# Kernel optimization log

Measured on AMD Instinct MI355X. Metric: run time of the kernel, lower is better.

The kernel has to match this reference:

```python
import jax, jax.numpy as jnp
import numpy as np

BN_EPS = 1e-5


def setup_inputs() -> dict:
    key = jax.random.key(0)
    ks = jax.random.split(key, 4)
    B, N, D = 8, 8192, 256
    outD = 256
    s = 1.0 / np.sqrt(D)
    return {
        "feature": jax.random.normal(ks[0], (B, N, D), dtype=jnp.float32),
        "W_qk": jax.random.normal(ks[1], (2, D, D), dtype=jnp.float32) * s,
        "b_qk": jnp.zeros((2, D), dtype=jnp.float32),
        "W_v": jax.random.normal(ks[2], (D, outD), dtype=jnp.float32) * s,
        "b_v": jnp.zeros((outD,), dtype=jnp.float32),
        "gamma": jnp.ones((D,), dtype=jnp.float32),
        "beta": jnp.zeros((D,), dtype=jnp.float32),
    }


def reference(feature, W_qk, b_qk, W_v, b_v, gamma, beta):
    # QK: [B, 2, N, D]
    QK = jnp.einsum("bnd,kde->bkne", feature, W_qk) + b_qk[None, :, None, :]
    # value: [B, N, outD]
    value = jnp.einsum("bnd,de->bne", feature, W_v) + b_v
    query = QK[:, 0]  # [B, N, D]
    key = QK[:, 1]    # [B, N, D]
    # softmax over the sequence axis (dim=1), per (batch, channel)
    sm = jax.nn.softmax(key, axis=1)
    # lambda context: softmax^T @ value -> [B, D, outD]
    lam = jnp.einsum("bnd,bne->bde", sm, value)
    # BatchNorm1d(featureDim) in training mode: channel axis = D (axis 1),
    # stats over (batch, spatial) = axes (0, 2); biased variance as torch uses.
    mean = jnp.mean(lam, axis=(0, 2), keepdims=True)
    var = jnp.var(lam, axis=(0, 2), keepdims=True)
    bn = (lam - mean) * jax.lax.rsqrt(var + BN_EPS)
    bn = bn * gamma[None, :, None] + beta[None, :, None]
    # result: query @ BN -> [B, N, outD]
    return jnp.einsum("bnd,bde->bne", query, bn)
```

## Files before the change

### kernel.cpp

```cpp
#include <hip/hip_runtime.h>

typedef unsigned short u16;
typedef __bf16 bf16x8 __attribute__((ext_vector_type(8)));
typedef float f32x4 __attribute__((ext_vector_type(4)));

#define LOG2E 1.44269504088896f

__device__ inline u16 f2b(float f) {
    unsigned u = __float_as_uint(f);
    u += 0x7fff + ((u >> 16) & 1);
    return (u16)(u >> 16);
}
__device__ inline float b2f(u16 u) { return __uint_as_float(((unsigned)u) << 16); }
__device__ inline unsigned pk2(float a, float b) {
    return (unsigned)f2b(a) | ((unsigned)f2b(b) << 16);
}
__device__ inline uint4 pack8(float4 a, float4 b) {
    return uint4{pk2(a.x, a.y), pk2(a.z, a.w), pk2(b.x, b.y), pk2(b.z, b.w)};
}

__device__ inline f32x4 mfma_bf16(uint4 a, uint4 b, f32x4 c) {
    return __builtin_amdgcn_mfma_f32_16x16x32_bf16(
        __builtin_bit_cast(bf16x8, a), __builtin_bit_cast(bf16x8, b), c, 0, 0, 0);
}

__global__ __launch_bounds__(256) void prep_w(const float* __restrict__ Wqk,
                                              const float* __restrict__ Wv,
                                              u16* __restrict__ WkT,
                                              u16* __restrict__ WvT,
                                              u16* __restrict__ Wqb) {
    int idx = blockIdx.x * 256 + threadIdx.x;
    int which = idx >> 16;
    int i = (idx >> 8) & 255;
    int j = idx & 255;
    if (which == 0)
        WkT[i * 256 + j] = f2b(Wqk[65536 + j * 256 + i]);
    else if (which == 1)
        WvT[i * 256 + j] = f2b(Wv[j * 256 + i]);
    else
        Wqb[i * 256 + j] = f2b(Wqk[i * 256 + j]);
}

__global__ __launch_bounds__(256) void gemm_kv(const float* __restrict__ A,
                                               const u16* __restrict__ BtK,
                                               const u16* __restrict__ BtV,
                                               const float* __restrict__ biasK,
                                               const float* __restrict__ biasV,
                                               u16* __restrict__ KT,
                                               u16* __restrict__ VT,
                                               u16* __restrict__ Xb) {
    __shared__ __align__(16) u16 lds[9216];
    u16* As = lds;
    u16* BsK = lds + 3072;
    u16* BsV = lds + 6144;

    const int t = threadIdx.x;
    const int c0 = blockIdx.x * 64;
    const int r0 = blockIdx.y * 64;

    const int tr = t >> 2;
    const int tk = (t & 3) * 8;
    const int w = t >> 6;
    const int lane = t & 63;
    const int l15 = lane & 15;
    const int q = lane >> 4;

    f32x4 accK[4], accV[4];
#pragma unroll
    for (int c = 0; c < 4; ++c) {
        accK[c] = f32x4{0.f, 0.f, 0.f, 0.f};
        accV[c] = f32x4{0.f, 0.f, 0.f, 0.f};
    }

    const float* Arow = A + (long)(r0 + tr) * 256 + tk;
    const u16* BrowK = BtK + (long)(c0 + tr) * 256 + tk;
    const u16* BrowV = BtV + (long)(c0 + tr) * 256 + tk;
    u16* AsW = &As[tr * 48 + tk];
    u16* BsWK = &BsK[tr * 48 + tk];
    u16* BsWV = &BsV[tr * 48 + tk];
    const u16* AsR = &As[(w * 16 + l15) * 48 + q * 8];
    const u16* BsRK = &BsK[l15 * 48 + q * 8];
    const u16* BsRV = &BsV[l15 * 48 + q * 8];
    const bool writeX = (Xb != nullptr) && (blockIdx.x == 0);
    u16* XbW = Xb + (long)(r0 + tr) * 256 + tk;

    float4 a0 = ((const float4*)Arow)[0];
    float4 a1 = ((const float4*)Arow)[1];
    uint4 bk = *(const uint4*)BrowK;
    uint4 bvv = *(const uint4*)BrowV;

    for (int k0 = 0; k0 < 256; k0 += 32) {
        uint4 ap = pack8(a0, a1);
        *(uint4*)AsW = ap;
        *(uint4*)BsWK = bk;
        *(uint4*)BsWV = bvv;
        if (writeX) *(uint4*)(XbW + k0) = ap;
        __syncthreads();
        if (k0 + 32 < 256) {
            a0 = ((const float4*)(Arow + k0 + 32))[0];
            a1 = ((const float4*)(Arow + k0 + 32))[1];
            bk = *(const uint4*)(BrowK + k0 + 32);
            bvv = *(const uint4*)(BrowV + k0 + 32);
        }
        uint4 af = *(const uint4*)AsR;
#pragma unroll
        for (int c = 0; c < 4; ++c) {
            uint4 bfK = *(const uint4*)(BsRK + c * 16 * 48);
            uint4 bfV = *(const uint4*)(BsRV + c * 16 * 48);
            accK[c] = mfma_bf16(af, bfK, accK[c]);
            accV[c] = mfma_bf16(af, bfV, accV[c]);
        }
        __syncthreads();
    }

    u16* Ct = lds;
    const int bb = r0 >> 13;
    const int n0 = r0 & 8191;
    const int cc = t >> 2;
    const int ng = (t & 3) * 16;
#pragma unroll
    for (int pass = 0; pass < 2; ++pass) {
        const f32x4* acc = pass ? accV : accK;
        const float* bias = pass ? biasV : biasK;
        u16* CT = pass ? VT : KT;
#pragma unroll
        for (int c = 0; c < 4; ++c) {
            float bv = bias[c0 + c * 16 + l15];
#pragma unroll
            for (int r = 0; r < 4; ++r) {
                Ct[(c * 16 + l15) * 72 + (w * 16 + q * 4 + r)] = f2b(acc[c][r] + bv);
            }
        }
        __syncthreads();
        long off = ((long)bb * 256 + (c0 + cc)) * 8192 + n0 + ng;
        uint4 v0 = *(uint4*)&Ct[cc * 72 + ng];
        uint4 v1 = *(uint4*)&Ct[cc * 72 + ng + 8];
        *(uint4*)(CT + off) = v0;
        *(uint4*)(CT + off + 8) = v1;
        __syncthreads();
    }
}

template <bool A_F32, bool OUT_F32, bool BIAS>
__global__ __launch_bounds__(256) void gemm_rowC(const void* __restrict__ Ain,
                                                 const u16* __restrict__ Bt,
                                                 const float* __restrict__ bias,
                                                 void* __restrict__ Cout,
                                                 int K, int rowsPerBatch, long btStride) {
    __shared__ __align__(16) u16 As[64 * 48];
    __shared__ __align__(16) u16 Bs[64 * 48];

    const int t = threadIdx.x;
    const int c0 = blockIdx.x * 64;
    const int r0 = blockIdx.y * 64;
    const int bb = r0 / rowsPerBatch;
    const u16* BtB = Bt + (long)bb * btStride;

    const int tr = t >> 2;
    const int tk = (t & 3) * 8;
    const int w = t >> 6;
    const int lane = t & 63;
    const int l15 = lane & 15;
    const int q = lane >> 4;

    f32x4 acc[4];
#pragma unroll
    for (int c = 0; c < 4; ++c) acc[c] = f32x4{0.f, 0.f, 0.f, 0.f};

    const float* ArowF = (const float*)Ain + (long)(r0 + tr) * K + tk;
    const u16* ArowB = (const u16*)Ain + (long)(r0 + tr) * K + tk;
    const u16* Brow = BtB + (long)(c0 + tr) * K + tk;
    u16* AsW = &As[tr * 48 + tk];
    u16* BsW = &Bs[tr * 48 + tk];
    const u16* AsR = &As[(w * 16 + l15) * 48 + q * 8];
    const u16* BsR = &Bs[l15 * 48 + q * 8];

    uint4 av;
    float4 a0, a1;
    if (A_F32) {
        a0 = ((const float4*)ArowF)[0];
        a1 = ((const float4*)ArowF)[1];
    } else {
        av = *(const uint4*)ArowB;
    }
    uint4 bv = *(const uint4*)Brow;

    for (int k0 = 0; k0 < K; k0 += 32) {
        *(uint4*)AsW = A_F32 ? pack8(a0, a1) : av;
        *(uint4*)BsW = bv;
        __syncthreads();
        if (k0 + 32 < K) {
            if (A_F32) {
                a0 = ((const float4*)(ArowF + k0 + 32))[0];
                a1 = ((const float4*)(ArowF + k0 + 32))[1];
            } else {
                av = *(const uint4*)(ArowB + k0 + 32);
            }
            bv = *(const uint4*)(Brow + k0 + 32);
        }
        uint4 af = *(const uint4*)AsR;
#pragma unroll
        for (int c = 0; c < 4; ++c) {
            uint4 bf = *(const uint4*)(BsR + c * 16 * 48);
            acc[c] = mfma_bf16(af, bf, acc[c]);
        }
        __syncthreads();
    }

#pragma unroll
    for (int c = 0; c < 4; ++c) {
        int col = c0 + c * 16 + l15;
        float bv2 = 0.f;
        if (BIAS) bv2 = bias[(long)bb * 256 + col];
#pragma unroll
        for (int r = 0; r < 4; ++r) {
            int row = r0 + w * 16 + q * 4 + r;
            float v = acc[c][r] + bv2;
            if (OUT_F32)
                ((float*)Cout)[(long)row * 256 + col] = v;
            else
                ((u16*)Cout)[(long)row * 256 + col] = f2b(v);
        }
    }
}

__global__ __launch_bounds__(256) void gemm_splitk(const u16* __restrict__ VT,
                                                   const u16* __restrict__ PT,
                                                   float* __restrict__ lamP,
                                                   int chunk) {
    __shared__ __align__(16) u16 As[64 * 48];
    __shared__ __align__(16) u16 Bs[64 * 48];

    const int t = threadIdx.x;
    const int c0 = blockIdx.x * 64;
    const int r0 = blockIdx.y * 64;
    const int s = blockIdx.z;
    const int bb = r0 >> 8;
    const long n0 = (long)s * chunk;

    const int tr = t >> 2;
    const int tk = (t & 3) * 8;
    const int w = t >> 6;
    const int lane = t & 63;
    const int l15 = lane & 15;
    const int q = lane >> 4;

    f32x4 acc[4];
#pragma unroll
    for (int c = 0; c < 4; ++c) acc[c] = f32x4{0.f, 0.f, 0.f, 0.f};

    const u16* Arow = VT + (long)(r0 + tr) * 8192 + n0 + tk;
    const u16* Brow = PT + ((long)bb * 256 + c0 + tr) * 8192 + n0 + tk;
    u16* AsW = &As[tr * 48 + tk];
    u16* BsW = &Bs[tr * 48 + tk];
    const u16* AsR = &As[(w * 16 + l15) * 48 + q * 8];
    const u16* BsR = &Bs[l15 * 48 + q * 8];

    uint4 av = *(const uint4*)Arow;
    uint4 bv = *(const uint4*)Brow;

    for (int k0 = 0; k0 < chunk; k0 += 32) {
        *(uint4*)AsW = av;
        *(uint4*)BsW = bv;
        __syncthreads();
        if (k0 + 32 < chunk) {
            av = *(const uint4*)(Arow + k0 + 32);
            bv = *(const uint4*)(Brow + k0 + 32);
        }
        uint4 af = *(const uint4*)AsR;
#pragma unroll
        for (int c = 0; c < 4; ++c) {
            uint4 bf = *(const uint4*)(BsR + c * 16 * 48);
            acc[c] = mfma_bf16(af, bf, acc[c]);
        }
        __syncthreads();
    }

    float* outp = lamP + (long)s * 524288;
#pragma unroll
    for (int c = 0; c < 4; ++c) {
        int col = c0 + c * 16 + l15;
#pragma unroll
        for (int r = 0; r < 4; ++r) {
            int row = r0 + w * 16 + q * 4 + r;
            outp[(long)row * 256 + col] = acc[c][r];
        }
    }
}

__global__ __launch_bounds__(256) void reduce_lam(const float* __restrict__ lamP,
                                                  float* __restrict__ lamT, int S) {
    int i = blockIdx.x * 256 + threadIdx.x;
    float4 v = ((const float4*)lamP)[i];
    for (int s = 1; s < S; ++s) {
        float4 p = ((const float4*)(lamP + (long)s * 524288))[i];
        v.x += p.x; v.y += p.y; v.z += p.z; v.w += p.w;
    }
    ((float4*)lamT)[i] = v;
}

__global__ __launch_bounds__(64) void softmax_rows(u16* __restrict__ KT) {
    const int row = blockIdx.x;
    const int lane = threadIdx.x;
    u16* p = KT + (long)row * 8192;

    uint4 buf[16];
#pragma unroll
    for (int i = 0; i < 16; ++i) buf[i] = *(const uint4*)(p + (i * 64 + lane) * 8);

    float m = -1e30f;
#pragma unroll
    for (int i = 0; i < 16; ++i) {
        const unsigned* u = (const unsigned*)&buf[i];
#pragma unroll
        for (int j = 0; j < 4; ++j) {
            m = fmaxf(m, fmaxf(b2f((u16)(u[j] & 0xffff)), b2f((u16)(u[j] >> 16))));
        }
    }
#pragma unroll
    for (int s = 32; s > 0; s >>= 1) m = fmaxf(m, __shfl_xor(m, s, 64));

    float sum = 0.f;
#pragma unroll
    for (int i = 0; i < 16; ++i) {
        const unsigned* u = (const unsigned*)&buf[i];
#pragma unroll
        for (int j = 0; j < 4; ++j) {
            sum += exp2f((b2f((u16)(u[j] & 0xffff)) - m) * LOG2E);
            sum += exp2f((b2f((u16)(u[j] >> 16)) - m) * LOG2E);
        }
    }
#pragma unroll
    for (int s = 32; s > 0; s >>= 1) sum += __shfl_xor(sum, s, 64);
    float rl = 1.0f / sum;

#pragma unroll
    for (int i = 0; i < 16; ++i) {
        unsigned* u = (unsigned*)&buf[i];
#pragma unroll
        for (int j = 0; j < 4; ++j) {
            float a = exp2f((b2f((u16)(u[j] & 0xffff)) - m) * LOG2E) * rl;
            float b = exp2f((b2f((u16)(u[j] >> 16)) - m) * LOG2E) * rl;
            u[j] = (unsigned)f2b(a) | ((unsigned)f2b(b) << 16);
        }
        *(uint4*)(p + (i * 64 + lane) * 8) = buf[i];
    }
}

__global__ __launch_bounds__(256) void bn_kernel(const float* __restrict__ lamT,
                                                 const float* __restrict__ gamma,
                                                 const float* __restrict__ beta,
                                                 u16* __restrict__ bnT) {
    const int d = blockIdx.x;
    const int t = threadIdx.x;
    float vals[8];
    float s = 0.f, ss = 0.f;
#pragma unroll
    for (int i = 0; i < 8; ++i) {
        float v = lamT[(long)(i * 256 + t) * 256 + d];
        vals[i] = v;
        s += v;
        ss += v * v;
    }
#pragma unroll
    for (int sh = 32; sh > 0; sh >>= 1) {
        s += __shfl_xor(s, sh, 64);
        ss += __shfl_xor(ss, sh, 64);
    }
    __shared__ float red[8];
    int w = t >> 6;
    if ((t & 63) == 0) {
        red[w] = s;
        red[w + 4] = ss;
    }
    __syncthreads();
    s = red[0] + red[1] + red[2] + red[3];
    ss = red[4] + red[5] + red[6] + red[7];
    float mean = s * (1.f / 2048.f);
    float var = ss * (1.f / 2048.f) - mean * mean;
    float scale = gamma[d] * rsqrtf(var + 1e-5f);
    float shift = beta[d] - mean * scale;
#pragma unroll
    for (int i = 0; i < 8; ++i)
        bnT[(long)(i * 256 + t) * 256 + d] = f2b(vals[i] * scale + shift);
}

__global__ __launch_bounds__(256) void outb_kernel(const float* __restrict__ bq,
                                                   const u16* __restrict__ bnT,
                                                   float* __restrict__ outb) {
    int b = blockIdx.x, e = threadIdx.x;
    const u16* rowp = bnT + ((long)b * 256 + e) * 256;
    float s = 0.f;
    for (int dd = 0; dd < 256; ++dd) s += bq[dd] * b2f(rowp[dd]);
    outb[b * 256 + e] = s;
}

extern "C" void kernel_launch(void* const* d_in, const int* in_sizes, int n_in,
                              void* d_out, int out_size, void* d_ws, size_t ws_size,
                              hipStream_t stream) {
    const float* feat = (const float*)d_in[0];
    const float* W_qk = (const float*)d_in[1];
    const float* b_qk = (const float*)d_in[2];
    const float* W_v = (const float*)d_in[3];
    const float* b_v = (const float*)d_in[4];
    const float* gamma = (const float*)d_in[5];
    const float* beta = (const float*)d_in[6];
    float* out = (float*)d_out;

    char* ws = (char*)d_ws;
    u16* KT = (u16*)(ws);
    u16* VT = (u16*)(ws + 33554432);
    u16* WkT = (u16*)(ws + 67108864);
    u16* WvT = (u16*)(ws + 67239936);
    u16* Wqb = (u16*)(ws + 67371008);
    const size_t base = 67502080;
    float* lamP = (float*)(ws + base);
    size_t avail = (ws_size > base) ? ws_size - base : 0;
    int S = (avail >= 8u * 2097152u) ? 8 : ((avail >= 4u * 2097152u) ? 4 : 2);
    u16* Xb = nullptr;
    if (avail >= (size_t)S * 2097152u + 33554432u) Xb = (u16*)(ws + base + (size_t)S * 2097152u);
    float* lamT = (float*)ws;
    u16* bnT = (u16*)(ws + 2097152);
    u16* WfoldT = (u16*)(ws + 3145728);
    float* outb = (float*)(ws + 4194304);

    prep_w<<<768, 256, 0, stream>>>(W_qk, W_v, WkT, WvT, Wqb);
    gemm_kv<<<dim3(4, 1024), 256, 0, stream>>>(feat, WkT, WvT, b_qk + 256, b_v, KT, VT, Xb);
    softmax_rows<<<2048, 64, 0, stream>>>(KT);
    gemm_splitk<<<dim3(4, 32, S), 256, 0, stream>>>(VT, KT, lamP, 8192 / S);
    reduce_lam<<<512, 256, 0, stream>>>(lamP, lamT, S);
    bn_kernel<<<256, 256, 0, stream>>>(lamT, gamma, beta, bnT);
    outb_kernel<<<8, 256, 0, stream>>>(b_qk, bnT, outb);
    gemm_rowC<false, false, false><<<dim3(4, 32), 256, 0, stream>>>(bnT, Wqb, nullptr,
                                                                    WfoldT, 256, 2048, 0L);
    if (Xb)
        gemm_rowC<false, true, true><<<dim3(4, 1024), 256, 0, stream>>>(Xb, WfoldT, outb, out,
                                                                        256, 8192, 65536L);
    else
        gemm_rowC<true, true, true><<<dim3(4, 1024), 256, 0, stream>>>(feat, WfoldT, outb, out,
                                                                       256, 8192, 65536L);
}
```

Baseline: 289.3 us.

## Widen GEMM tiles to full 256 columns and load B tiles via global_load_lds

Several GEMM kernels are restructured at once. gemm_kv and gemm_out now give each block all 256 output columns, so the fp32 feature rows are read and packed once instead of four times, and the bf16 Xb copy is dropped. gemm_splitk moves to 128x128 tiles with more split-K slices, and B tiles (and A tiles where already bf16) are loaded straight into LDS with global_load_lds. The trade is much higher register pressure (32 accumulator vectors in gemm_kv), unpadded LDS rows that may cause bank conflicts, and a larger partial-sum buffer to reduce.

```diff
diff --git a/kernel.cpp b/kernel.cpp
--- a/kernel.cpp
+++ b/kernel.cpp
@@ -18,10 +18,14 @@
 __device__ inline uint4 pack8(float4 a, float4 b) {
     return uint4{pk2(a.x, a.y), pk2(a.z, a.w), pk2(b.x, b.y), pk2(b.z, b.w)};
 }
-
 __device__ inline f32x4 mfma_bf16(uint4 a, uint4 b, f32x4 c) {
     return __builtin_amdgcn_mfma_f32_16x16x32_bf16(
         __builtin_bit_cast(bf16x8, a), __builtin_bit_cast(bf16x8, b), c, 0, 0, 0);
+}
+__device__ inline void ld16(const u16* g, u16* l) {
+    __builtin_amdgcn_global_load_lds(
+        (const __attribute__((address_space(1))) unsigned int*)g,
+        (__attribute__((address_space(3))) unsigned int*)l, 16, 0, 0);
 }
 
 __global__ __launch_bounds__(256) void prep_w(const float* __restrict__ Wqk,
@@ -41,251 +45,202 @@
         Wqb[i * 256 + j] = f2b(Wqk[i * 256 + j]);
 }
 
-__global__ __launch_bounds__(256) void gemm_kv(const float* __restrict__ A,
-                                               const u16* __restrict__ BtK,
-                                               const u16* __restrict__ BtV,
-                                               const float* __restrict__ biasK,
-                                               const float* __restrict__ biasV,
-                                               u16* __restrict__ KT,
-                                               u16* __restrict__ VT,
-                                               u16* __restrict__ Xb) {
-    __shared__ __align__(16) u16 lds[9216];
+__global__ __launch_bounds__(256, 2) void gemm_kv(const float* __restrict__ A,
+                                                  const u16* __restrict__ BtK,
+                                                  const u16* __restrict__ BtV,
+                                                  const float* __restrict__ biasK,
+                                                  const float* __restrict__ biasV,
+                                                  u16* __restrict__ KT,
+                                                  u16* __restrict__ VT) {
+    __shared__ __align__(16) u16 lds[18432];
     u16* As = lds;
-    u16* BsK = lds + 3072;
-    u16* BsV = lds + 6144;
+    u16* BsK = lds + 2048;
+    u16* BsV = lds + 10240;
 
     const int t = threadIdx.x;
-    const int c0 = blockIdx.x * 64;
-    const int r0 = blockIdx.y * 64;
-
-    const int tr = t >> 2;
-    const int tk = (t & 3) * 8;
-    const int w = t >> 6;
-    const int lane = t & 63;
-    const int l15 = lane & 15;
-    const int q = lane >> 4;
-
-    f32x4 accK[4], accV[4];
-#pragma unroll
-    for (int c = 0; c < 4; ++c) {
+    const int r0 = blockIdx.x * 64;
+    const int w = t >> 6, lane = t & 63, l15 = lane & 15, q = lane >> 4;
+
+    f32x4 accK[16], accV[16];
+#pragma unroll
+    for (int c = 0; c < 16; ++c) {
         accK[c] = f32x4{0.f, 0.f, 0.f, 0.f};
         accV[c] = f32x4{0.f, 0.f, 0.f, 0.f};
     }
 
-    const float* Arow = A + (long)(r0 + tr) * 256 + tk;
-    const u16* BrowK = BtK + (long)(c0 + tr) * 256 + tk;
-    const u16* BrowV = BtV + (long)(c0 + tr) * 256 + tk;
-    u16* AsW = &As[tr * 48 + tk];
-    u16* BsWK = &BsK[tr * 48 + tk];
-    u16* BsWV = &BsV[tr * 48 + tk];
-    const u16* AsR = &As[(w * 16 + l15) * 48 + q * 8];
-    const u16* BsRK = &BsK[l15 * 48 + q * 8];
-    const u16* BsRV = &BsV[l15 * 48 + q * 8];
-    const bool writeX = (Xb != nullptr) && (blockIdx.x == 0);
-    u16* XbW = Xb + (long)(r0 + tr) * 256 + tk;
+    const int ar = t >> 2;
+    const int ak = (t & 3) * 8;
+    const float* Arow = A + (long)(r0 + ar) * 256 + ak;
+    u16* AsW = As + t * 8;
 
     float4 a0 = ((const float4*)Arow)[0];
     float4 a1 = ((const float4*)Arow)[1];
-    uint4 bk = *(const uint4*)BrowK;
-    uint4 bvv = *(const uint4*)BrowV;
 
     for (int k0 = 0; k0 < 256; k0 += 32) {
-        uint4 ap = pack8(a0, a1);
-        *(uint4*)AsW = ap;
-        *(uint4*)BsWK = bk;
-        *(uint4*)BsWV = bvv;
-        if (writeX) *(uint4*)(XbW + k0) = ap;
+#pragma unroll
+        for (int j = 0; j < 4; ++j) {
+            int ch = j * 256 + t;
+            int br = ch >> 2;
+            int bk = (ch & 3) * 8;
+            ld16(BtK + br * 256 + k0 + bk, BsK + j * 2048 + w * 512);
+            ld16(BtV + br * 256 + k0 + bk, BsV + j * 2048 + w * 512);
+        }
+        *(uint4*)AsW = pack8(a0, a1);
         __syncthreads();
         if (k0 + 32 < 256) {
             a0 = ((const float4*)(Arow + k0 + 32))[0];
             a1 = ((const float4*)(Arow + k0 + 32))[1];
-            bk = *(const uint4*)(BrowK + k0 + 32);
-            bvv = *(const uint4*)(BrowV + k0 + 32);
-        }
-        uint4 af = *(const uint4*)AsR;
-#pragma unroll
-        for (int c = 0; c < 4; ++c) {
-            uint4 bfK = *(const uint4*)(BsRK + c * 16 * 48);
-            uint4 bfV = *(const uint4*)(BsRV + c * 16 * 48);
-            accK[c] = mfma_bf16(af, bfK, accK[c]);
-            accV[c] = mfma_bf16(af, bfV, accV[c]);
-        }
-        __syncthreads();
-    }
-
+        }
+        uint4 af = *(const uint4*)(As + (w * 16 + l15) * 32 + q * 8);
+#pragma unroll
+        for (int c = 0; c < 16; ++c) {
+            uint4 bK = *(const uint4*)(BsK + (c * 16 + l15) * 32 + q * 8);
+            uint4 bV = *(const uint4*)(BsV + (c * 16 + l15) * 32 + q * 8);
+            accK[c] = mfma_bf16(af, bK, accK[c]);
+            accV[c] = mfma_bf16(af, bV, accV[c]);
+        }
+        __syncthreads();
+    }
+
+    const int bb = r0 >> 13, n0 = r0 & 8191;
     u16* Ct = lds;
-    const int bb = r0 >> 13;
-    const int n0 = r0 & 8191;
-    const int cc = t >> 2;
-    const int ng = (t & 3) * 16;
 #pragma unroll
     for (int pass = 0; pass < 2; ++pass) {
         const f32x4* acc = pass ? accV : accK;
         const float* bias = pass ? biasV : biasK;
         u16* CT = pass ? VT : KT;
 #pragma unroll
-        for (int c = 0; c < 4; ++c) {
-            float bv = bias[c0 + c * 16 + l15];
-#pragma unroll
-            for (int r = 0; r < 4; ++r) {
-                Ct[(c * 16 + l15) * 72 + (w * 16 + q * 4 + r)] = f2b(acc[c][r] + bv);
-            }
-        }
-        __syncthreads();
-        long off = ((long)bb * 256 + (c0 + cc)) * 8192 + n0 + ng;
-        uint4 v0 = *(uint4*)&Ct[cc * 72 + ng];
-        uint4 v1 = *(uint4*)&Ct[cc * 72 + ng + 8];
-        *(uint4*)(CT + off) = v0;
-        *(uint4*)(CT + off + 8) = v1;
-        __syncthreads();
-    }
-}
-
-template <bool A_F32, bool OUT_F32, bool BIAS>
-__global__ __launch_bounds__(256) void gemm_rowC(const void* __restrict__ Ain,
-                                                 const u16* __restrict__ Bt,
-                                                 const float* __restrict__ bias,
-                                                 void* __restrict__ Cout,
-                                                 int K, int rowsPerBatch, long btStride) {
-    __shared__ __align__(16) u16 As[64 * 48];
-    __shared__ __align__(16) u16 Bs[64 * 48];
+        for (int c = 0; c < 16; ++c) {
+            float bv = bias[c * 16 + l15];
+            ushort4 pk;
+            pk.x = f2b(acc[c][0] + bv);
+            pk.y = f2b(acc[c][1] + bv);
+            pk.z = f2b(acc[c][2] + bv);
+            pk.w = f2b(acc[c][3] + bv);
+            *(ushort4*)&Ct[(c * 16 + l15) * 72 + w * 16 + q * 4] = pk;
+        }
+        __syncthreads();
+        long off = ((long)bb * 256 + t) * 8192 + n0;
+#pragma unroll
+        for (int j = 0; j < 8; ++j)
+            *(uint4*)(CT + off + j * 8) = *(const uint4*)&Ct[t * 72 + j * 8];
+        __syncthreads();
+    }
+}
+
+__global__ __launch_bounds__(256, 3) void gemm_out(const float* __restrict__ A,
+                                                   const u16* __restrict__ WfoldT,
+                                                   const float* __restrict__ outb,
+                                                   float* __restrict__ C) {
+    __shared__ __align__(16) u16 lds[10240];
+    u16* As = lds;
+    u16* Bs = lds + 2048;
 
     const int t = threadIdx.x;
-    const int c0 = blockIdx.x * 64;
-    const int r0 = blockIdx.y * 64;
-    const int bb = r0 / rowsPerBatch;
-    const u16* BtB = Bt + (long)bb * btStride;
-
-    const int tr = t >> 2;
-    const int tk = (t & 3) * 8;
-    const int w = t >> 6;
-    const int lane = t & 63;
-    const int l15 = lane & 15;
-    const int q = lane >> 4;
-
-    f32x4 acc[4];
-#pragma unroll
-    for (int c = 0; c < 4; ++c) acc[c] = f32x4{0.f, 0.f, 0.f, 0.f};
-
-    const float* ArowF = (const float*)Ain + (long)(r0 + tr) * K + tk;
-    const u16* ArowB = (const u16*)Ain + (long)(r0 + tr) * K + tk;
-    const u16* Brow = BtB + (long)(c0 + tr) * K + tk;
-    u16* AsW = &As[tr * 48 + tk];
-    u16* BsW = &Bs[tr * 48 + tk];
-    const u16* AsR = &As[(w * 16 + l15) * 48 + q * 8];
-    const u16* BsR = &Bs[l15 * 48 + q * 8];
-
-    uint4 av;
-    float4 a0, a1;
-    if (A_F32) {
-        a0 = ((const float4*)ArowF)[0];
-        a1 = ((const float4*)ArowF)[1];
-    } else {
-        av = *(const uint4*)ArowB;
-    }
-    uint4 bv = *(const uint4*)Brow;
-
-    for (int k0 = 0; k0 < K; k0 += 32) {
-        *(uint4*)AsW = A_F32 ? pack8(a0, a1) : av;
-        *(uint4*)BsW = bv;
-        __syncthreads();
-        if (k0 + 32 < K) {
-            if (A_F32) {
-                a0 = ((const float4*)(ArowF + k0 + 32))[0];
-                a1 = ((const float4*)(ArowF + k0 + 32))[1];
-            } else {
-                av = *(const uint4*)(ArowB + k0 + 32);
-            }
-            bv = *(const uint4*)(Brow + k0 + 32);
-        }
-        uint4 af = *(const uint4*)AsR;
-#pragma unroll
-        for (int c = 0; c < 4; ++c) {
-            uint4 bf = *(const uint4*)(BsR + c * 16 * 48);
+    const int r0 = blockIdx.x * 64;
+    const int bb = r0 >> 13;
+    const int w = t >> 6, lane = t & 63, l15 = lane & 15, q = lane >> 4;
+    const u16* Bt = WfoldT + (long)bb * 65536;
+
+    f32x4 acc[16];
+#pragma unroll
+    for (int c = 0; c < 16; ++c) acc[c] = f32x4{0.f, 0.f, 0.f, 0.f};
+
+    const float* Arow = A + (long)(r0 + (t >> 2)) * 256 + (t & 3) * 8;
+    u16* AsW = As + t * 8;
+
+    float4 a0 = ((const float4*)Arow)[0];
+    float4 a1 = ((const float4*)Arow)[1];
+
+    for (int k0 = 0; k0 < 256; k0 += 32) {
+#pragma unroll
+        for (int j = 0; j < 4; ++j) {
+            int ch = j * 256 + t;
+            ld16(Bt + (ch >> 2) * 256 + k0 + (ch & 3) * 8, Bs + j * 2048 + w * 512);
+        }
+        *(uint4*)AsW = pack8(a0, a1);
+        __syncthreads();
+        if (k0 + 32 < 256) {
+            a0 = ((const float4*)(Arow + k0 + 32))[0];
+            a1 = ((const float4*)(Arow + k0 + 32))[1];
+        }
+        uint4 af = *(const uint4*)(As + (w * 16 + l15) * 32 + q * 8);
+#pragma unroll
+        for (int c = 0; c < 16; ++c) {
+            uint4 bf = *(const uint4*)(Bs + (c * 16 + l15) * 32 + q * 8);
             acc[c] = mfma_bf16(af, bf, acc[c]);
         }
         __syncthreads();
     }
 
 #pragma unroll
-    for (int c = 0; c < 4; ++c) {
-        int col = c0 + c * 16 + l15;
-        float bv2 = 0.f;
-        if (BIAS) bv2 = bias[(long)bb * 256 + col];
+    for (int c = 0; c < 16; ++c) {
+        int col = c * 16 + l15;
+        float bv = outb[bb * 256 + col];
 #pragma unroll
         for (int r = 0; r < 4; ++r) {
             int row = r0 + w * 16 + q * 4 + r;
-            float v = acc[c][r] + bv2;
-            if (OUT_F32)
-                ((float*)Cout)[(long)row * 256 + col] = v;
-            else
-                ((u16*)Cout)[(long)row * 256 + col] = f2b(v);
-        }
-    }
-}
-
-__global__ __launch_bounds__(256) void gemm_splitk(const u16* __restrict__ VT,
-                                                   const u16* __restrict__ PT,
-                                                   float* __restrict__ lamP,
-                                                   int chunk) {
-    __shared__ __align__(16) u16 As[64 * 48];
-    __shared__ __align__(16) u16 Bs[64 * 48];
+            C[(long)row * 256 + col] = acc[c][r] + bv;
+        }
+    }
+}
+
+__global__ __launch_bounds__(256, 4) void gemm_splitk(const u16* __restrict__ VT,
+                                                      const u16* __restrict__ PT,
+                                                      float* __restrict__ lamP,
+                                                      int chunk) {
+    __shared__ __align__(16) u16 lds[8192];
+    u16* As = lds;
+    u16* Bs = lds + 4096;
 
     const int t = threadIdx.x;
-    const int c0 = blockIdx.x * 64;
-    const int r0 = blockIdx.y * 64;
+    const int r0 = blockIdx.x * 128;
+    const int c0 = blockIdx.y * 128;
     const int s = blockIdx.z;
-    const int bb = r0 >> 8;
+    const int bb = blockIdx.x >> 1;
     const long n0 = (long)s * chunk;
-
-    const int tr = t >> 2;
-    const int tk = (t & 3) * 8;
-    const int w = t >> 6;
-    const int lane = t & 63;
-    const int l15 = lane & 15;
-    const int q = lane >> 4;
-
-    f32x4 acc[4];
-#pragma unroll
-    for (int c = 0; c < 4; ++c) acc[c] = f32x4{0.f, 0.f, 0.f, 0.f};
-
-    const u16* Arow = VT + (long)(r0 + tr) * 8192 + n0 + tk;
-    const u16* Brow = PT + ((long)bb * 256 + c0 + tr) * 8192 + n0 + tk;
-    u16* AsW = &As[tr * 48 + tk];
-    u16* BsW = &Bs[tr * 48 + tk];
-    const u16* AsR = &As[(w * 16 + l15) * 48 + q * 8];
-    const u16* BsR = &Bs[l15 * 48 + q * 8];
-
-    uint4 av = *(const uint4*)Arow;
-    uint4 bv = *(const uint4*)Brow;
+    const int w = t >> 6, lane = t & 63, l15 = lane & 15, q = lane >> 4;
+
+    f32x4 acc[2][8];
+#pragma unroll
+    for (int rt = 0; rt < 2; ++rt)
+#pragma unroll
+        for (int c = 0; c < 8; ++c) acc[rt][c] = f32x4{0.f, 0.f, 0.f, 0.f};
 
     for (int k0 = 0; k0 < chunk; k0 += 32) {
-        *(uint4*)AsW = av;
-        *(uint4*)BsW = bv;
-        __syncthreads();
-        if (k0 + 32 < chunk) {
-            av = *(const uint4*)(Arow + k0 + 32);
-            bv = *(const uint4*)(Brow + k0 + 32);
-        }
-        uint4 af = *(const uint4*)AsR;
-#pragma unroll
-        for (int c = 0; c < 4; ++c) {
-            uint4 bf = *(const uint4*)(BsR + c * 16 * 48);
-            acc[c] = mfma_bf16(af, bf, acc[c]);
+#pragma unroll
+        for (int j = 0; j < 2; ++j) {
+            int ch = j * 256 + t;
+            int br = ch >> 2;
+            int bk = (ch & 3) * 8;
+            ld16(VT + (long)(r0 + br) * 8192 + n0 + k0 + bk, As + j * 2048 + w * 512);
+            ld16(PT + ((long)bb * 256 + c0 + br) * 8192 + n0 + k0 + bk,
+                 Bs + j * 2048 + w * 512);
+        }
+        __syncthreads();
+        uint4 af0 = *(const uint4*)(As + (w * 32 + l15) * 32 + q * 8);
+        uint4 af1 = *(const uint4*)(As + (w * 32 + 16 + l15) * 32 + q * 8);
+#pragma unroll
+        for (int c = 0; c < 8; ++c) {
+            uint4 bf = *(const uint4*)(Bs + (c * 16 + l15) * 32 + q * 8);
+            acc[0][c] = mfma_bf16(af0, bf, acc[0][c]);
+            acc[1][c] = mfma_bf16(af1, bf, acc[1][c]);
         }
         __syncthreads();
     }
 
     float* outp = lamP + (long)s * 524288;
 #pragma unroll
-    for (int c = 0; c < 4; ++c) {
-        int col = c0 + c * 16 + l15;
-#pragma unroll
-        for (int r = 0; r < 4; ++r) {
-            int row = r0 + w * 16 + q * 4 + r;
-            outp[(long)row * 256 + col] = acc[c][r];
-        }
-    }
+    for (int rt = 0; rt < 2; ++rt)
+#pragma unroll
+        for (int c = 0; c < 8; ++c) {
+            int col = c0 + c * 16 + l15;
+#pragma unroll
+            for (int r = 0; r < 4; ++r) {
+                int row = r0 + w * 32 + rt * 16 + q * 4 + r;
+                outp[(long)row * 256 + col] = acc[rt][c][r];
+            }
+        }
 }
 
 __global__ __launch_bounds__(256) void reduce_lam(const float* __restrict__ lamP,
@@ -297,6 +252,49 @@
         v.x += p.x; v.y += p.y; v.z += p.z; v.w += p.w;
     }
     ((float4*)lamT)[i] = v;
+}
+
+__global__ __launch_bounds__(256, 4) void gemm_fold(const u16* __restrict__ Abn,
+                                                    const u16* __restrict__ Wqb,
+                                                    u16* __restrict__ WfoldT) {
+    __shared__ __align__(16) u16 lds[4096];
+    u16* As = lds;
+    u16* Bs = lds + 2048;
+
+    const int t = threadIdx.x;
+    const int r0 = blockIdx.x * 64;
+    const int c0 = blockIdx.y * 64;
+    const int w = t >> 6, lane = t & 63, l15 = lane & 15, q = lane >> 4;
+
+    f32x4 acc[4];
+#pragma unroll
+    for (int c = 0; c < 4; ++c) acc[c] = f32x4{0.f, 0.f, 0.f, 0.f};
+
+    const int br = t >> 2;
+    const int bk = (t & 3) * 8;
+
+    for (int k0 = 0; k0 < 256; k0 += 32) {
+        ld16(Abn + (long)(r0 + br) * 256 + k0 + bk, As + w * 512);
+        ld16(Wqb + (long)(c0 + br) * 256 + k0 + bk, Bs + w * 512);
+        __syncthreads();
+        uint4 af = *(const uint4*)(As + (w * 16 + l15) * 32 + q * 8);
+#pragma unroll
+        for (int c = 0; c < 4; ++c) {
+            uint4 bf = *(const uint4*)(Bs + (c * 16 + l15) * 32 + q * 8);
+            acc[c] = mfma_bf16(af, bf, acc[c]);
+        }
+        __syncthreads();
+    }
+
+#pragma unroll
+    for (int c = 0; c < 4; ++c) {
+        int col = c0 + c * 16 + l15;
+#pragma unroll
+        for (int r = 0; r < 4; ++r) {
+            int row = r0 + w * 16 + q * 4 + r;
+            WfoldT[(long)row * 256 + col] = f2b(acc[c][r]);
+        }
+    }
 }
 
 __global__ __launch_bounds__(64) void softmax_rows(u16* __restrict__ KT) {
@@ -416,27 +414,21 @@
     const size_t base = 67502080;
     float* lamP = (float*)(ws + base);
     size_t avail = (ws_size > base) ? ws_size - base : 0;
-    int S = (avail >= 8u * 2097152u) ? 8 : ((avail >= 4u * 2097152u) ? 4 : 2);
-    u16* Xb = nullptr;
-    if (avail >= (size_t)S * 2097152u + 33554432u) Xb = (u16*)(ws + base + (size_t)S * 2097152u);
+    int S = (avail >= 16u * 2097152u) ? 16
+          : (avail >= 8u * 2097152u) ? 8
+          : (avail >= 4u * 2097152u) ? 4 : 2;
     float* lamT = (float*)ws;
     u16* bnT = (u16*)(ws + 2097152);
     u16* WfoldT = (u16*)(ws + 3145728);
     float* outb = (float*)(ws + 4194304);
 
     prep_w<<<768, 256, 0, stream>>>(W_qk, W_v, WkT, WvT, Wqb);
-    gemm_kv<<<dim3(4, 1024), 256, 0, stream>>>(feat, WkT, WvT, b_qk + 256, b_v, KT, VT, Xb);
+    gemm_kv<<<1024, 256, 0, stream>>>(feat, WkT, WvT, b_qk + 256, b_v, KT, VT);
     softmax_rows<<<2048, 64, 0, stream>>>(KT);
-    gemm_splitk<<<dim3(4, 32, S), 256, 0, stream>>>(VT, KT, lamP, 8192 / S);
+    gemm_splitk<<<dim3(16, 2, S), 256, 0, stream>>>(VT, KT, lamP, 8192 / S);
     reduce_lam<<<512, 256, 0, stream>>>(lamP, lamT, S);
     bn_kernel<<<256, 256, 0, stream>>>(lamT, gamma, beta, bnT);
     outb_kernel<<<8, 256, 0, stream>>>(b_qk, bnT, outb);
-    gemm_rowC<false, false, false><<<dim3(4, 32), 256, 0, stream>>>(bnT, Wqb, nullptr,
-                                                                    WfoldT, 256, 2048, 0L);
-    if (Xb)
-        gemm_rowC<false, true, true><<<dim3(4, 1024), 256, 0, stream>>>(Xb, WfoldT, outb, out,
-                                                                        256, 8192, 65536L);
-    else
-        gemm_rowC<true, true, true><<<dim3(4, 1024), 256, 0, stream>>>(feat, WfoldT, outb, out,
-                                                                       256, 8192, 65536L);
-}
+    gemm_fold<<<dim3(32, 4), 256, 0, stream>>>(bnT, Wqb, WfoldT);
+    gemm_out<<<1024, 256, 0, stream>>>(feat, WfoldT, outb, out);
+}
```

Measured after the change: 253.2 us. 1.14x faster.
